# Performance work log

Measured on AMD Instinct MI355X. Metric: run time of the kernel, lower is better.

The kernel has to match this reference:

```python
import jax, jax.numpy as jnp
import numpy as np

N_NODES = 50000
N_EDGES = 1_600_000
N_REL = 8
D_IN = 128
D_OUT = 128


def _unique_edges(rng, n_nodes, n_rel, n_edges):
    # Torch module clamps the dense adjacency to 0/1, so duplicate
    # (rel, src, dst) triples collapse; generate unique edges so the
    # edge-list formulation matches exactly.
    m = 2 * n_edges
    src = rng.integers(0, n_nodes, m)
    dst = rng.integers(0, n_nodes, m)
    et = rng.integers(0, n_rel, m)
    key = (et.astype(np.int64) * n_nodes + src) * n_nodes + dst
    _, idx = np.unique(key, return_index=True)
    idx = np.sort(idx)[:n_edges]
    return src[idx], dst[idx], et[idx]


def setup_inputs() -> dict:
    key = jax.random.key(0)
    kx, kw, kr, kb = jax.random.split(key, 4)
    rng = np.random.default_rng(0)
    src, dst, et = _unique_edges(rng, N_NODES, N_REL, N_EDGES)
    bound = 1.0 / np.sqrt(D_OUT)
    return {
        "x": jax.random.normal(kx, (N_NODES, D_IN), dtype=jnp.float32),
        "edge_index": jnp.asarray(np.stack([src, dst]), dtype=jnp.int64),
        "edge_type": jnp.asarray(et, dtype=jnp.int64),
        "weight": jax.random.uniform(kw, (N_REL, D_OUT, D_IN), minval=-bound, maxval=bound, dtype=jnp.float32),
        "root": jax.random.uniform(kr, (D_OUT, D_IN), minval=-bound, maxval=bound, dtype=jnp.float32),
        "bias": jax.random.uniform(kb, (D_OUT,), minval=-bound, maxval=bound, dtype=jnp.float32),
    }


def reference(x, edge_index, edge_type, weight, root, bias):
    # Math identical to: adj[l, src, dst] = 1; adj row-normalized (mean);
    # out = sum_r norm_adj_r @ x @ W_r^T + x @ root^T + bias.
    n_rel, d_out, d_in = weight.shape
    n_nodes = x.shape[0]
    src = edge_index[0]
    dst = edge_index[1]
    seg = (edge_type * n_nodes + src).astype(jnp.int32)  # segment per (rel, node)
    num_seg = n_rel * n_nodes
    # sum of neighbor features per (relation, node): [R*N, d_in]
    agg = jax.ops.segment_sum(x[dst], seg, num_segments=num_seg)
    deg = jax.ops.segment_sum(jnp.ones((src.shape[0],), dtype=x.dtype), seg, num_segments=num_seg)
    norm = jnp.where(deg > 0, 1.0 / deg, 0.0)[:, None]  # mean aggr, nan_to_num(0)
    agg = (agg * norm).reshape(n_rel, n_nodes, d_in)
    out = jnp.einsum('rnd,rod->no', agg, weight)
    out = out + x @ root.T + bias[None]
    return out
```

## Files before the change

kernel.cpp:

```cpp
#include <hip/hip_runtime.h>


#define D 128
#define SCAN_CHUNK 2048
#define SEG_BITS 9
#define SEGS_PER_BUCKET 512
#define NBLK 256
#define NDEG 32

typedef __attribute__((ext_vector_type(8))) short short8;
typedef __attribute__((ext_vector_type(4))) float v4f;
typedef __attribute__((ext_vector_type(2))) float f32x2;
typedef __attribute__((ext_vector_type(4))) unsigned uint4v;

#define GLOAD_LDS16(gptr, lptr) \
    __builtin_amdgcn_global_load_lds((const __attribute__((address_space(1))) void*)(gptr), \
                                     (__attribute__((address_space(3))) void*)(lptr), 16, 0, 0)

__device__ __forceinline__ unsigned short f2b(float f) {
    union { float f; unsigned u; } v; v.f = f;
    unsigned r = v.u + 0x7fffu + ((v.u >> 16) & 1u);
    return (unsigned short)(r >> 16);
}
__device__ __forceinline__ float blo(unsigned u) {
    union { unsigned u; float f; } v; v.u = u << 16; return v.f;
}
__device__ __forceinline__ float bhi(unsigned u) {
    union { unsigned u; float f; } v; v.u = u & 0xffff0000u; return v.f;
}

__global__ __launch_bounds__(256)
void histA_cvt(const int* __restrict__ ei, const int* __restrict__ et,
               int* __restrict__ blockHist, int nE, int nN, int B, int epb,
               const float* __restrict__ x, long long nx,
               const float* __restrict__ w, long long nw,
               const float* __restrict__ root, long long nr,
               unsigned short* __restrict__ Abuf,
               unsigned short* __restrict__ wB, size_t SLs) {
    __shared__ int lh[1024];
    const int tid = threadIdx.x;
    if (blockIdx.x >= NBLK) {
        long long i = ((long long)(blockIdx.x - NBLK) * blockDim.x + tid) * 4;
        if (i < nx) {
            float4 v = *(const float4*)(x + i);
            uint2 p;
            p.x = (unsigned)f2b(v.x) | ((unsigned)f2b(v.y) << 16);
            p.y = (unsigned)f2b(v.z) | ((unsigned)f2b(v.w) << 16);
            long long n = i >> 7;
            int d = (int)(i & 127);
            size_t o = (size_t)((d >> 5) * 9 + 8) * SLs + (size_t)n * 32 + (d & 31);
            *(uint2*)(Abuf + o) = p;
            return;
        }
        const float* src;
        unsigned short* dst;
        long long j;
        if (i < nx + nw) { src = w; dst = wB; j = i - nx; }
        else if (i < nx + nw + nr) { src = root; dst = wB + nw; j = i - nx - nw; }
        else return;
        float4 v = *(const float4*)(src + j);
        uint2 p;
        p.x = (unsigned)f2b(v.x) | ((unsigned)f2b(v.y) << 16);
        p.y = (unsigned)f2b(v.z) | ((unsigned)f2b(v.w) << 16);
        *(uint2*)(dst + j) = p;
        return;
    }
    for (int b = tid; b < B; b += 256) lh[b] = 0;
    __syncthreads();
    const int base = blockIdx.x * epb;
    const int lim = min(base + epb, nE);
    for (int e = base + tid * 4; e < lim; e += 1024) {
        if (e + 4 <= lim) {
            int4 s = *(const int4*)(ei + e);
            int4 t = *(const int4*)(et + e);
            atomicAdd(&lh[(t.x * nN + s.x) >> SEG_BITS], 1);
            atomicAdd(&lh[(t.y * nN + s.y) >> SEG_BITS], 1);
            atomicAdd(&lh[(t.z * nN + s.z) >> SEG_BITS], 1);
            atomicAdd(&lh[(t.w * nN + s.w) >> SEG_BITS], 1);
        } else {
            for (int k = e; k < lim; k++)
                atomicAdd(&lh[(et[k] * nN + ei[k]) >> SEG_BITS], 1);
        }
    }
    __syncthreads();
    for (int b = tid; b < B; b += 256)
        blockHist[b * NBLK + blockIdx.x] = lh[b];
}

__global__ __launch_bounds__(256)
void scan1(const int* __restrict__ in, int* __restrict__ excl,
           int* __restrict__ blockSums, int n) {
    __shared__ int t[256];
    const int tid = threadIdx.x;
    const int base = blockIdx.x * SCAN_CHUNK + tid * 8;
    int v[8];
    int tot = 0;
#pragma unroll
    for (int i = 0; i < 8; i++) {
        v[i] = (base + i < n) ? in[base + i] : 0;
        tot += v[i];
    }
    t[tid] = tot;
    __syncthreads();
    for (int off = 1; off < 256; off <<= 1) {
        int add = (tid >= off) ? t[tid - off] : 0;
        __syncthreads();
        t[tid] += add;
        __syncthreads();
    }
    int run = t[tid] - tot;
#pragma unroll
    for (int i = 0; i < 8; i++) {
        if (base + i < n) excl[base + i] = run;
        run += v[i];
    }
    if (tid == 255) blockSums[blockIdx.x] = t[255];
}

__global__ __launch_bounds__(256)
void scatterA(const int* __restrict__ ei, const int* __restrict__ et,
              const int* __restrict__ scanned, const int* __restrict__ blockSums,
              unsigned* __restrict__ bucketEdges,
              int nE, int nN, int B, int epb, int nSB) {
    __shared__ int cur[1024];
    __shared__ int bs[128];
    const int tid = threadIdx.x;
    int myv = 0;
    if (tid < 128) { myv = (tid < nSB) ? blockSums[tid] : 0; bs[tid] = myv; }
    __syncthreads();
    for (int o = 1; o < 128; o <<= 1) {
        int add = (tid >= o && tid < 128) ? bs[tid - o] : 0;
        __syncthreads();
        if (tid < 128) bs[tid] += add;
        __syncthreads();
    }
    if (tid < 128) bs[tid] -= myv;
    __syncthreads();
    for (int b = tid; b < B; b += 256) {
        int idx = b * NBLK + blockIdx.x;
        cur[b] = scanned[idx] + bs[idx >> 11];
    }
    __syncthreads();
    const int base = blockIdx.x * epb;
    const int lim = min(base + epb, nE);
    for (int e = base + tid * 4; e < lim; e += 1024) {
        if (e + 4 <= lim) {
            int4 s = *(const int4*)(ei + e);
            int4 t = *(const int4*)(et + e);
            int4 d = *(const int4*)(ei + nE + e);
            int sg;
            sg = t.x * nN + s.x;
            bucketEdges[atomicAdd(&cur[sg >> SEG_BITS], 1)] =
                ((unsigned)(sg & (SEGS_PER_BUCKET - 1)) << 16) | (unsigned)d.x;
            sg = t.y * nN + s.y;
            bucketEdges[atomicAdd(&cur[sg >> SEG_BITS], 1)] =
                ((unsigned)(sg & (SEGS_PER_BUCKET - 1)) << 16) | (unsigned)d.y;
            sg = t.z * nN + s.z;
            bucketEdges[atomicAdd(&cur[sg >> SEG_BITS], 1)] =
                ((unsigned)(sg & (SEGS_PER_BUCKET - 1)) << 16) | (unsigned)d.z;
            sg = t.w * nN + s.w;
            bucketEdges[atomicAdd(&cur[sg >> SEG_BITS], 1)] =
                ((unsigned)(sg & (SEGS_PER_BUCKET - 1)) << 16) | (unsigned)d.w;
        } else {
            for (int k = e; k < lim; k++) {
                int sg = et[k] * nN + ei[k];
                bucketEdges[atomicAdd(&cur[sg >> SEG_BITS], 1)] =
                    ((unsigned)(sg & (SEGS_PER_BUCKET - 1)) << 16) | (unsigned)ei[nE + k];
            }
        }
    }
}

__global__ __launch_bounds__(256)
void segOff(const unsigned* __restrict__ bucketEdges, const int* __restrict__ scanned,
            const int* __restrict__ blockSums,
            int4* __restrict__ permRec, unsigned short* __restrict__ sortedDst,
            int* __restrict__ permMax, int nE, int numSeg, int B, int nSB) {
    __shared__ int lh[SEGS_PER_BUCKET];
    __shared__ int sc[256];
    __shared__ int lcur[SEGS_PER_BUCKET];
    __shared__ int dcnt[256];
    __shared__ int dbase[256];
    __shared__ int smax[32];
    __shared__ int bs[128];
    const int tid = threadIdx.x;
    const int b = blockIdx.x;
    int myv = 0;
    if (tid < 128) { myv = (tid < nSB) ? blockSums[tid] : 0; bs[tid] = myv; }
    lh[2 * tid] = 0; lh[2 * tid + 1] = 0;
    dcnt[tid] = 0;
    if (tid < 32) smax[tid] = 0;
    __syncthreads();
    for (int o = 1; o < 128; o <<= 1) {
        int add = (tid >= o && tid < 128) ? bs[tid - o] : 0;
        __syncthreads();
        if (tid < 128) bs[tid] += add;
        __syncthreads();
    }
    if (tid < 128) bs[tid] -= myv;
    __syncthreads();
    const int i0 = b * NBLK;
    const int eBase = scanned[i0] + bs[i0 >> 11];
    int eEnd = nE;
    if (b + 1 < B) {
        const int i1 = (b + 1) * NBLK;
        eEnd = scanned[i1] + bs[i1 >> 11];
    }
    const int segBase = b * SEGS_PER_BUCKET;
    const int segLim = min(SEGS_PER_BUCKET, numSeg - segBase);

    for (int i = eBase + tid; i < eEnd; i += 256)
        atomicAdd(&lh[bucketEdges[i] >> 16], 1);
    __syncthreads();
    const int li0 = 2 * tid, li1 = 2 * tid + 1;
    const int sub = li0 >> 6;
    int a0 = lh[li0], a1 = lh[li1];
    int b0 = min(a0, NDEG - 1), b1 = min(a1, NDEG - 1), r0 = 0, r1 = 0;
    if (li0 < segLim) r0 = atomicAdd(&dcnt[sub * NDEG + b0], 1);
    if (li1 < segLim) r1 = atomicAdd(&dcnt[sub * NDEG + b1], 1);
    sc[tid] = a0 + a1;
    __syncthreads();
    for (int o = 1; o < 256; o <<= 1) {
        int add = (tid >= o) ? sc[tid - o] : 0;
        __syncthreads();
        sc[tid] += add;
        __syncthreads();
    }
    int pairBase = sc[tid] - (a0 + a1);
    int g0 = eBase + pairBase;
    int g1 = g0 + a0;
    lcur[li0] = g0;
    lcur[li1] = g1;
    if (tid < 8) {
        int run = 0;
#pragma unroll
        for (int k = 0; k < NDEG; k++) { dbase[tid * NDEG + k] = run; run += dcnt[tid * NDEG + k]; }
    }
    __syncthreads();
    if (li0 < segLim) {
        int rk = dbase[sub * NDEG + b0] + r0;
        permRec[segBase + sub * 64 + rk] = make_int4(g0, a0, segBase + li0, 0);
        atomicMax(&smax[(sub << 2) + (rk >> 4)], a0);
    }
    if (li1 < segLim) {
        int rk = dbase[sub * NDEG + b1] + r1;
        permRec[segBase + sub * 64 + rk] = make_int4(g1, a1, segBase + li1, 0);
        atomicMax(&smax[(sub << 2) + (rk >> 4)], a1);
    }
    for (int i = eBase + tid; i < eEnd; i += 256) {
        unsigned u = bucketEdges[i];
        int pos = atomicAdd(&lcur[u >> 16], 1);
        sortedDst[pos] = (unsigned short)(u & 0xFFFFu);
    }
    __syncthreads();
    if (tid < 32) permMax[b * 32 + tid] = smax[tid];
}

__global__ __launch_bounds__(256)
void rgcn_gather(const unsigned short* __restrict__ Abase,
                 const unsigned short* __restrict__ sortedDst,
                 const int4* __restrict__ permRec,
                 const int* __restrict__ permMax,
                 unsigned short* __restrict__ Abuf, int nN, int numSeg,
                 size_t SLs, unsigned long long M) {
    const int tid = threadIdx.x;
    const int lane = tid & 63;
    const int idx4 = lane & 3;
    const int grp = lane >> 2;
    const int wv = tid >> 6;
    const int gsi0 = blockIdx.x * 128 + wv * 32 + grp;
    const int gsi1 = gsi0 + 16;
    const int sl = blockIdx.y;
    const bool v0 = (gsi0 < numSeg);
    const bool v1 = (gsi1 < numSeg);

    int4 rc0 = v0 ? permRec[gsi0] : make_int4(0, 0, 0, 0);
    int4 rc1 = v1 ? permRec[gsi1] : make_int4(0, 0, 0, 0);
    int mx0 = v0 ? permMax[gsi0 >> 4] : 0;
    int mx1 = v1 ? permMax[gsi1 >> 4] : 0;
    mx0 = __builtin_amdgcn_readfirstlane(mx0);
    mx1 = __builtin_amdgcn_readfirstlane(mx1);

    const int start0 = rc0.x, cnt0 = v0 ? rc0.y : 0, seg0 = rc0.z;
    const int start1 = rc1.x, cnt1 = v1 ? rc1.y : 0, seg1 = rc1.z;

    f32x2 a0[4], a1[4];
#pragma unroll
    for (int i = 0; i < 4; i++) { a0[i] = (f32x2){0.f, 0.f}; a1[i] = (f32x2){0.f, 0.f}; }

    const unsigned short* xSlab = Abase + (size_t)(sl * 9 + 8) * SLs + idx4 * 8;

    const int mxm = max(mx0, mx1);
    for (int b = 0; b < mxm; b += 4) {
        uint4v w0[4], w1[4];
        int myD0 = 0, myD1 = 0;
        if (b < mx0) myD0 = (b + idx4 < cnt0) ? (int)sortedDst[start0 + b + idx4] : 0;
        if (b < mx1) myD1 = (b + idx4 < cnt1) ? (int)sortedDst[start1 + b + idx4] : 0;
        if (b < mx0) {
#pragma unroll
            for (int j = 0; j < 4; j++) {
                int dst = __shfl(myD0, grp * 4 + j);
                bool act = (b + j < cnt0);
                w0[j] = act ? *(const uint4v*)(xSlab + ((size_t)dst << 5))
                            : (uint4v){0u, 0u, 0u, 0u};
            }
        }
        if (b < mx1) {
#pragma unroll
            for (int j = 0; j < 4; j++) {
                int dst = __shfl(myD1, grp * 4 + j);
                bool act = (b + j < cnt1);
                w1[j] = act ? *(const uint4v*)(xSlab + ((size_t)dst << 5))
                            : (uint4v){0u, 0u, 0u, 0u};
            }
        }
        if (b < mx0) {
#pragma unroll
            for (int j = 0; j < 4; j++) {
                f32x2 t0 = (f32x2){blo(w0[j].x), bhi(w0[j].x)};
                f32x2 t1 = (f32x2){blo(w0[j].y), bhi(w0[j].y)};
                f32x2 t2 = (f32x2){blo(w0[j].z), bhi(w0[j].z)};
                f32x2 t3 = (f32x2){blo(w0[j].w), bhi(w0[j].w)};
                asm("v_pk_add_f32 %0, %0, %1" : "+v"(a0[0]) : "v"(t0));
                asm("v_pk_add_f32 %0, %0, %1" : "+v"(a0[1]) : "v"(t1));
                asm("v_pk_add_f32 %0, %0, %1" : "+v"(a0[2]) : "v"(t2));
                asm("v_pk_add_f32 %0, %0, %1" : "+v"(a0[3]) : "v"(t3));
            }
        }
        if (b < mx1) {
#pragma unroll
            for (int j = 0; j < 4; j++) {
                f32x2 t0 = (f32x2){blo(w1[j].x), bhi(w1[j].x)};
                f32x2 t1 = (f32x2){blo(w1[j].y), bhi(w1[j].y)};
                f32x2 t2 = (f32x2){blo(w1[j].z), bhi(w1[j].z)};
                f32x2 t3 = (f32x2){blo(w1[j].w), bhi(w1[j].w)};
                asm("v_pk_add_f32 %0, %0, %1" : "+v"(a1[0]) : "v"(t0));
                asm("v_pk_add_f32 %0, %0, %1" : "+v"(a1[1]) : "v"(t1));
                asm("v_pk_add_f32 %0, %0, %1" : "+v"(a1[2]) : "v"(t2));
                asm("v_pk_add_f32 %0, %0, %1" : "+v"(a1[3]) : "v"(t3));
            }
        }
    }

    if (v0) {
        float s = cnt0 > 0 ? 1.0f / (float)cnt0 : 0.f;
        const int r = (int)(((unsigned long long)seg0 * M) >> 48);
        const int n = seg0 - r * nN;
        unsigned p0, p1, p2, p3;
        float e0, e1;
        e0 = a0[0].x * s; e1 = a0[0].y * s;
        asm("v_cvt_pk_bf16_f32 %0, %1, %2" : "=v"(p0) : "v"(e0), "v"(e1));
        e0 = a0[1].x * s; e1 = a0[1].y * s;
        asm("v_cvt_pk_bf16_f32 %0, %1, %2" : "=v"(p1) : "v"(e0), "v"(e1));
        e0 = a0[2].x * s; e1 = a0[2].y * s;
        asm("v_cvt_pk_bf16_f32 %0, %1, %2" : "=v"(p2) : "v"(e0), "v"(e1));
        e0 = a0[3].x * s; e1 = a0[3].y * s;
        asm("v_cvt_pk_bf16_f32 %0, %1, %2" : "=v"(p3) : "v"(e0), "v"(e1));
        uint4v pkt = (uint4v){p0, p1, p2, p3};
        __builtin_nontemporal_store(pkt,
            (uint4v*)(Abuf + (size_t)(sl * 9 + r) * SLs + (size_t)n * 32 + idx4 * 8));
    }
    if (v1) {
        float s = cnt1 > 0 ? 1.0f / (float)cnt1 : 0.f;
        const int r = (int)(((unsigned long long)seg1 * M) >> 48);
        const int n = seg1 - r * nN;
        unsigned p0, p1, p2, p3;
        float e0, e1;
        e0 = a1[0].x * s; e1 = a1[0].y * s;
        asm("v_cvt_pk_bf16_f32 %0, %1, %2" : "=v"(p0) : "v"(e0), "v"(e1));
        e0 = a1[1].x * s; e1 = a1[1].y * s;
        asm("v_cvt_pk_bf16_f32 %0, %1, %2" : "=v"(p1) : "v"(e0), "v"(e1));
        e0 = a1[2].x * s; e1 = a1[2].y * s;
        asm("v_cvt_pk_bf16_f32 %0, %1, %2" : "=v"(p2) : "v"(e0), "v"(e1));
        e0 = a1[3].x * s; e1 = a1[3].y * s;
        asm("v_cvt_pk_bf16_f32 %0, %1, %2" : "=v"(p3) : "v"(e0), "v"(e1));
        uint4v pkt = (uint4v){p0, p1, p2, p3};
        __builtin_nontemporal_store(pkt,
            (uint4v*)(Abuf + (size_t)(sl * 9 + r) * SLs + (size_t)n * 32 + idx4 * 8));
    }
}

__global__ __launch_bounds__(256)
void rgcn_gemm_mfma(const unsigned short* __restrict__ A,
                    const unsigned short* __restrict__ wB,
                    const float* __restrict__ bias,
                    float* __restrict__ out, int nN, int nRel, size_t SLs) {
    __shared__ __align__(16) unsigned short As[2][128 * 64];
    __shared__ __align__(16) unsigned short Bs[2][128 * 64];
    const int tid = threadIdx.x;
    const int wave = tid >> 6;
    const int lane = tid & 63;
    const int wm = wave & 1;
    const int wn = wave >> 1;
    const int m16 = lane & 15;
    const int q = lane >> 4;
    const int row0 = blockIdx.x * 128;

    v4f acc[4][4];
#pragma unroll
    for (int i = 0; i < 4; i++)
#pragma unroll
        for (int j = 0; j < 4; j++) acc[i][j] = (v4f){0.f, 0.f, 0.f, 0.f};

    const int sw = m16 & 7;
    int aoff[4][2], boff[4][2];
#pragma unroll
    for (int mt = 0; mt < 4; mt++) {
        int row = wm * 64 + mt * 16 + m16;
#pragma unroll
        for (int kb = 0; kb < 2; kb++)
            aoff[mt][kb] = row * 64 + (((kb * 4 + q) ^ sw) * 8);
    }
#pragma unroll
    for (int nt = 0; nt < 4; nt++) {
        int o = wn * 64 + nt * 16 + m16;
#pragma unroll
        for (int kb = 0; kb < 2; kb++)
            boff[nt][kb] = o * 64 + (((kb * 4 + q) ^ sw) * 8);
    }

    const int l8 = lane >> 3;
    const int gd = (lane & 7) ^ l8;
    size_t aB[4];
#pragma unroll
    for (int i = 0; i < 4; i++)
        aB[i] = (size_t)((gd >> 2) * 9) * SLs
              + (size_t)(row0 + wave * 32 + i * 8 + l8) * 32 + (gd & 3) * 8;
    const size_t bBase = (size_t)(wave * 32 + l8) * D + gd * 8;

    const int nT = 2 * (nRel + 1);

#define STAGE(buf, t) do { \
        const int s_ = (t) >> 1, h_ = (t) & 1; \
        const size_t hs_ = (size_t)h_ * 18 * SLs + (size_t)s_ * SLs; \
        const unsigned short* gb_ = wB + (size_t)s_ * (D * D) + h_ * 64 + bBase; \
        GLOAD_LDS16(A + aB[0] + hs_, &As[buf][(wave * 4 + 0) * 512]); \
        GLOAD_LDS16(A + aB[1] + hs_, &As[buf][(wave * 4 + 1) * 512]); \
        GLOAD_LDS16(A + aB[2] + hs_, &As[buf][(wave * 4 + 2) * 512]); \
        GLOAD_LDS16(A + aB[3] + hs_, &As[buf][(wave * 4 + 3) * 512]); \
        GLOAD_LDS16(gb_,        &Bs[buf][(wave * 4 + 0) * 512]); \
        GLOAD_LDS16(gb_ + 1024, &Bs[buf][(wave * 4 + 1) * 512]); \
        GLOAD_LDS16(gb_ + 2048, &Bs[buf][(wave * 4 + 2) * 512]); \
        GLOAD_LDS16(gb_ + 3072, &Bs[buf][(wave * 4 + 3) * 512]); \
    } while (0)

    STAGE(0, 0);
    int cur = 0;
    for (int t = 0; t < nT; ++t) {
        if (t + 1 < nT) {
            STAGE(cur ^ 1, t + 1);
            asm volatile("s_waitcnt vmcnt(8)" ::: "memory");
        } else {
            asm volatile("s_waitcnt vmcnt(0)" ::: "memory");
        }
        __builtin_amdgcn_s_barrier();
        __builtin_amdgcn_sched_barrier(0);
        const unsigned short* Ab = As[cur];
        const unsigned short* Bb = Bs[cur];
#pragma unroll
        for (int kb = 0; kb < 2; kb++) {
            short8 a[4], b[4];
#pragma unroll
            for (int mt = 0; mt < 4; mt++)
                a[mt] = *(const short8*)&Ab[aoff[mt][kb]];
#pragma unroll
            for (int nt = 0; nt < 4; nt++)
                b[nt] = *(const short8*)&Bb[boff[nt][kb]];
#pragma unroll
            for (int mt = 0; mt < 4; mt++)
#pragma unroll
                for (int nt = 0; nt < 4; nt++)
                    acc[mt][nt] = __builtin_amdgcn_mfma_f32_16x16x32_bf16(
                        a[mt], b[nt], acc[mt][nt], 0, 0, 0);
        }
        asm volatile("s_waitcnt lgkmcnt(0)" ::: "memory");
        __builtin_amdgcn_s_barrier();
        __builtin_amdgcn_sched_barrier(0);
        cur ^= 1;
    }
#undef STAGE

#pragma unroll
    for (int mt = 0; mt < 4; mt++) {
#pragma unroll
        for (int nt = 0; nt < 4; nt++) {
            int col = wn * 64 + nt * 16 + m16;
            float bi = bias[col];
#pragma unroll
            for (int reg = 0; reg < 4; reg++) {
                int rrow = row0 + wm * 64 + mt * 16 + q * 4 + reg;
                if (rrow < nN)
                    out[(size_t)rrow * D + col] = acc[mt][nt][reg] + bi;
            }
        }
    }
}

extern "C" void kernel_launch(void* const* d_in, const int* in_sizes, int n_in,
                              void* d_out, int out_size, void* d_ws, size_t ws_size,
                              hipStream_t stream) {
    const float* x    = (const float*)d_in[0];
    const int*   ei   = (const int*)d_in[1];
    const int*   et   = (const int*)d_in[2];
    const float* w    = (const float*)d_in[3];
    const float* root = (const float*)d_in[4];
    const float* bias = (const float*)d_in[5];
    float* out = (float*)d_out;

    const int nN   = in_sizes[0] / D;
    const int nE   = in_sizes[2];
    const int nRel = in_sizes[3] / (D * D);
    const int numSeg = nRel * nN;
    const int B = (numSeg + SEGS_PER_BUCKET - 1) >> SEG_BITS;
    const int nBH = B * NBLK;
    const int epb = (((nE + NBLK - 1) / NBLK) + 3) & ~3;
    const int nNalloc = (nN + 127) & ~127;
    const size_t SLs = (size_t)nNalloc * 32;
    const unsigned long long M = ((1ULL << 48) + nN - 1) / nN;

    char* p = (char*)d_ws;
    unsigned* bucketEdges   = (unsigned*)p;        p += (size_t)nE * sizeof(unsigned);
    unsigned short* sortedDst = (unsigned short*)p; p += (size_t)nE * sizeof(unsigned short);
    p = (char*)(((uintptr_t)p + 255) & ~(uintptr_t)255);
    int* blockHist = (int*)p;  p += (size_t)nBH * sizeof(int);
    int* scanned   = (int*)p;  p += (size_t)nBH * sizeof(int);
    int* blockSums = (int*)p;  p += 256 * sizeof(int);
    p = (char*)(((uintptr_t)p + 255) & ~(uintptr_t)255);
    int4* permRec  = (int4*)p; p += (size_t)numSeg * sizeof(int4);
    int* permMax   = (int*)p;  p += (size_t)B * 32 * sizeof(int);
    p = (char*)(((uintptr_t)p + 255) & ~(uintptr_t)255);
    unsigned short* wBc  = (unsigned short*)p;  p += (size_t)(nRel + 1) * D * D * sizeof(unsigned short);
    p = (char*)(((uintptr_t)p + 255) & ~(uintptr_t)255);
    unsigned short* Abuf = (unsigned short*)p;

    const int nScanBlocks = (nBH + SCAN_CHUNK - 1) / SCAN_CHUNK;

    long long nx = (long long)nN * D;
    long long nw = (long long)nRel * D * D;
    long long nr = (long long)D * D;
    long long ncvt = (nx + nw + nr) / 4;
    const int nCvtBlk = (int)((ncvt + 255) / 256);

    histA_cvt<<<NBLK + nCvtBlk, 256, 0, stream>>>(ei, et, blockHist, nE, nN, B, epb,
                                                  x, nx, w, nw, root, nr, Abuf, wBc, SLs);
    scan1<<<nScanBlocks, 256, 0, stream>>>(blockHist, scanned, blockSums, nBH);
    scatterA<<<NBLK, 256, 0, stream>>>(ei, et, scanned, blockSums, bucketEdges,
                                       nE, nN, B, epb, nScanBlocks);
    segOff<<<B, 256, 0, stream>>>(bucketEdges, scanned, blockSums, permRec, sortedDst, permMax,
                                  nE, numSeg, B, nScanBlocks);

    dim3 gg((numSeg + 127) / 128, 4);
    rgcn_gather<<<gg, 256, 0, stream>>>(Abuf, sortedDst, permRec, permMax, Abuf,
                                        nN, numSeg, SLs, M);

    rgcn_gemm_mfma<<<(nN + 127) / 128, 256, 0, stream>>>(Abuf, wBc, bias, out, nN, nRel, SLs);
}
```

Before: 228.3 us.

## Replace LDS double-buffered GEMM with direct global-to-register MFMA operand loads

Rewrites the final GEMM so each wave loads its A and B MFMA fragments straight from global memory into registers, dropping the LDS staging, double buffering and per-step barriers. The loop is fully unrolled through a template for the common 18-step case, launch bounds ask for two blocks per CU, and output stores become nontemporal. The aim is to remove barrier and LDS round-trip overhead. In exchange, operands that other waves share are fetched again from L2/global (B especially), and full unrolling may raise register pressure.

```diff
diff --git a/kernel.cpp b/kernel.cpp
--- a/kernel.cpp
+++ b/kernel.cpp
@@ -12,10 +12,6 @@
 typedef __attribute__((ext_vector_type(4))) float v4f;
 typedef __attribute__((ext_vector_type(2))) float f32x2;
 typedef __attribute__((ext_vector_type(4))) unsigned uint4v;
-
-#define GLOAD_LDS16(gptr, lptr) \
-    __builtin_amdgcn_global_load_lds((const __attribute__((address_space(1))) void*)(gptr), \
-                                     (__attribute__((address_space(3))) void*)(lptr), 16, 0, 0)
 
 __device__ __forceinline__ unsigned short f2b(float f) {
     union { float f; unsigned u; } v; v.f = f;
@@ -380,13 +376,12 @@
     }
 }
 
-__global__ __launch_bounds__(256)
-void rgcn_gemm_mfma(const unsigned short* __restrict__ A,
-                    const unsigned short* __restrict__ wB,
-                    const float* __restrict__ bias,
-                    float* __restrict__ out, int nN, int nRel, size_t SLs) {
-    __shared__ __align__(16) unsigned short As[2][128 * 64];
-    __shared__ __align__(16) unsigned short Bs[2][128 * 64];
+template<int NT>
+__global__ __launch_bounds__(256, 2)
+void rgcn_gemm_direct(const unsigned short* __restrict__ A,
+                      const unsigned short* __restrict__ wB,
+                      const float* __restrict__ bias,
+                      float* __restrict__ out, int nN, size_t SLs, int nTr) {
     const int tid = threadIdx.x;
     const int wave = tid >> 6;
     const int lane = tid & 63;
@@ -402,83 +397,39 @@
 #pragma unroll
         for (int j = 0; j < 4; j++) acc[i][j] = (v4f){0.f, 0.f, 0.f, 0.f};
 
-    const int sw = m16 & 7;
-    int aoff[4][2], boff[4][2];
-#pragma unroll
-    for (int mt = 0; mt < 4; mt++) {
-        int row = wm * 64 + mt * 16 + m16;
+    size_t rowA[4], rowB[4];
+#pragma unroll
+    for (int mt = 0; mt < 4; mt++)
+        rowA[mt] = (size_t)(row0 + wm * 64 + mt * 16 + m16) * 32 + q * 8;
+#pragma unroll
+    for (int nt = 0; nt < 4; nt++)
+        rowB[nt] = (size_t)(wn * 64 + nt * 16 + m16) * D + q * 8;
+
+    const int nT = NT ? NT : nTr;
+#pragma unroll
+    for (int t = 0; t < nT; ++t) {
+        const int s_ = t >> 1, h_ = t & 1;
+        short8 a[4][2], b[4][2];
+#pragma unroll
+        for (int kb = 0; kb < 2; kb++) {
+            const unsigned short* Ab = A + (size_t)((h_ * 2 + kb) * 9 + s_) * SLs;
+#pragma unroll
+            for (int mt = 0; mt < 4; mt++)
+                a[mt][kb] = *(const short8*)(Ab + rowA[mt]);
+            const unsigned short* Bb = wB + (size_t)s_ * (D * D) + h_ * 64 + kb * 32;
+#pragma unroll
+            for (int nt = 0; nt < 4; nt++)
+                b[nt][kb] = *(const short8*)(Bb + rowB[nt]);
+        }
 #pragma unroll
         for (int kb = 0; kb < 2; kb++)
-            aoff[mt][kb] = row * 64 + (((kb * 4 + q) ^ sw) * 8);
-    }
-#pragma unroll
-    for (int nt = 0; nt < 4; nt++) {
-        int o = wn * 64 + nt * 16 + m16;
-#pragma unroll
-        for (int kb = 0; kb < 2; kb++)
-            boff[nt][kb] = o * 64 + (((kb * 4 + q) ^ sw) * 8);
-    }
-
-    const int l8 = lane >> 3;
-    const int gd = (lane & 7) ^ l8;
-    size_t aB[4];
-#pragma unroll
-    for (int i = 0; i < 4; i++)
-        aB[i] = (size_t)((gd >> 2) * 9) * SLs
-              + (size_t)(row0 + wave * 32 + i * 8 + l8) * 32 + (gd & 3) * 8;
-    const size_t bBase = (size_t)(wave * 32 + l8) * D + gd * 8;
-
-    const int nT = 2 * (nRel + 1);
-
-#define STAGE(buf, t) do { \
-        const int s_ = (t) >> 1, h_ = (t) & 1; \
-        const size_t hs_ = (size_t)h_ * 18 * SLs + (size_t)s_ * SLs; \
-        const unsigned short* gb_ = wB + (size_t)s_ * (D * D) + h_ * 64 + bBase; \
-        GLOAD_LDS16(A + aB[0] + hs_, &As[buf][(wave * 4 + 0) * 512]); \
-        GLOAD_LDS16(A + aB[1] + hs_, &As[buf][(wave * 4 + 1) * 512]); \
-        GLOAD_LDS16(A + aB[2] + hs_, &As[buf][(wave * 4 + 2) * 512]); \
-        GLOAD_LDS16(A + aB[3] + hs_, &As[buf][(wave * 4 + 3) * 512]); \
-        GLOAD_LDS16(gb_,        &Bs[buf][(wave * 4 + 0) * 512]); \
-        GLOAD_LDS16(gb_ + 1024, &Bs[buf][(wave * 4 + 1) * 512]); \
-        GLOAD_LDS16(gb_ + 2048, &Bs[buf][(wave * 4 + 2) * 512]); \
-        GLOAD_LDS16(gb_ + 3072, &Bs[buf][(wave * 4 + 3) * 512]); \
-    } while (0)
-
-    STAGE(0, 0);
-    int cur = 0;
-    for (int t = 0; t < nT; ++t) {
-        if (t + 1 < nT) {
-            STAGE(cur ^ 1, t + 1);
-            asm volatile("s_waitcnt vmcnt(8)" ::: "memory");
-        } else {
-            asm volatile("s_waitcnt vmcnt(0)" ::: "memory");
-        }
-        __builtin_amdgcn_s_barrier();
-        __builtin_amdgcn_sched_barrier(0);
-        const unsigned short* Ab = As[cur];
-        const unsigned short* Bb = Bs[cur];
-#pragma unroll
-        for (int kb = 0; kb < 2; kb++) {
-            short8 a[4], b[4];
-#pragma unroll
-            for (int mt = 0; mt < 4; mt++)
-                a[mt] = *(const short8*)&Ab[aoff[mt][kb]];
-#pragma unroll
-            for (int nt = 0; nt < 4; nt++)
-                b[nt] = *(const short8*)&Bb[boff[nt][kb]];
 #pragma unroll
             for (int mt = 0; mt < 4; mt++)
 #pragma unroll
                 for (int nt = 0; nt < 4; nt++)
                     acc[mt][nt] = __builtin_amdgcn_mfma_f32_16x16x32_bf16(
-                        a[mt], b[nt], acc[mt][nt], 0, 0, 0);
-        }
-        asm volatile("s_waitcnt lgkmcnt(0)" ::: "memory");
-        __builtin_amdgcn_s_barrier();
-        __builtin_amdgcn_sched_barrier(0);
-        cur ^= 1;
-    }
-#undef STAGE
+                        a[mt][kb], b[nt][kb], acc[mt][nt], 0, 0, 0);
+    }
 
 #pragma unroll
     for (int mt = 0; mt < 4; mt++) {
@@ -490,7 +441,8 @@
             for (int reg = 0; reg < 4; reg++) {
                 int rrow = row0 + wm * 64 + mt * 16 + q * 4 + reg;
                 if (rrow < nN)
-                    out[(size_t)rrow * D + col] = acc[mt][nt][reg] + bi;
+                    __builtin_nontemporal_store(acc[mt][nt][reg] + bi,
+                        &out[(size_t)rrow * D + col]);
             }
         }
     }
@@ -553,5 +505,10 @@
     rgcn_gather<<<gg, 256, 0, stream>>>(Abuf, sortedDst, permRec, permMax, Abuf,
                                         nN, numSeg, SLs, M);
 
-    rgcn_gemm_mfma<<<(nN + 127) / 128, 256, 0, stream>>>(Abuf, wBc, bias, out, nN, nRel, SLs);
-}
+    const int nT = 2 * (nRel + 1);
+    const int gemmBlocks = (nN + 127) / 128;
+    if (nT == 18)
+        rgcn_gemm_direct<18><<<gemmBlocks, 256, 0, stream>>>(Abuf, wBc, bias, out, nN, SLs, nT);
+    else
+        rgcn_gemm_direct<0><<<gemmBlocks, 256, 0, stream>>>(Abuf, wBc, bias, out, nN, SLs, nT);
+}
```

Result: slower. 284.5 us (+24.6%).
